# Performance work log

Measured on AMD Instinct MI355X. Metric: run time of the kernel, lower is better.

## Reference

```python
import jax, jax.numpy as jnp
import numpy as np

N = 100000      # n_nodes
D = 64          # in_features == out_features (elementwise W mul requires equality)
DEG = 16        # avg degree for random edges
H = 2           # n_head
ALPHA = 0.2     # LeakyReLU negative slope


def setup_inputs() -> dict:
    key = jax.random.key(0)
    k1, k2, k3 = jax.random.split(key, 3)
    inputs = jax.random.normal(k1, (N, D), dtype=jnp.float32)
    # random edges + self-loops so every row has at least one edge (nonzero rowsum)
    rnd = jax.random.randint(k2, (2, N * DEG), 0, N)
    self_loops = jnp.tile(jnp.arange(N)[None, :], (2, 1))
    edge_index = jnp.concatenate([self_loops, rnd], axis=1)  # [2, 1.7M]
    # per-head params, matching torch init: W = ones, a ~ U(-stdv, stdv)
    W = jnp.ones((H, D), dtype=jnp.float32)
    stdv = 1.0 / np.sqrt(D * 2)
    a = jax.random.uniform(k3, (H, 2 * D), dtype=jnp.float32, minval=-stdv, maxval=stdv)
    return {"inputs": inputs, "edge_index": edge_index, "W": W, "a": a}


def reference(inputs, edge_index, W, a):
    n = inputs.shape[0]
    row, col = edge_index[0], edge_index[1]

    def head(Wh, ah):
        h = inputs * Wh  # [N, D]
        # a @ [h_src; h_dst] decomposes into per-node dots, then scalar edge gather
        score = (h @ ah[:D])[row] + (h @ ah[D:])[col]          # [E]
        e = jnp.exp(jnp.where(score > 0, score, ALPHA * score))  # exp(leaky_relu)
        rowsum = jax.ops.segment_sum(e, row, num_segments=n)     # [N]
        # sparse.mm(coo(edge, e), inputs): h_prime[i] = sum_j e_ij * inputs[j]
        h_prime = jax.ops.segment_sum(e[:, None] * inputs[col], row, num_segments=n)
        return h_prime / rowsum[:, None]

    outs = jax.vmap(head)(W, a)  # [H, N, D]
    return outs.mean(axis=0)
```

## Files before the change

kernel.cpp:

```cpp
#include <hip/hip_runtime.h>


#define D 64
#define ALPHA 0.2f
#define CAP 96
#define BSHIFT 9
#define BROWS 512
#define MAXBUK 256
#define TILE 2048
#define PACKSHIFT 23
#define COLMASK ((1u << PACKSHIFT) - 1u)

__device__ __forceinline__ unsigned bf16rne(float f) {
    unsigned u = __float_as_uint(f);
    u += 0x7fffu + ((u >> 16) & 1u);
    return u >> 16;
}

__global__ __launch_bounds__(256) void k_scores_cast(
    const float* __restrict__ x, const float* __restrict__ W,
    const float* __restrict__ a, float4* __restrict__ s,
    unsigned short* __restrict__ xh, int N)
{
    int wid  = (blockIdx.x * blockDim.x + threadIdx.x) >> 6;
    int lane = threadIdx.x & 63;
    if (wid >= N) return;
    float v = x[(size_t)wid * D + lane];
    xh[(size_t)wid * D + lane] = (unsigned short)bf16rne(v);
    float h0 = v * W[lane];
    float h1 = v * W[D + lane];
    float t0 = h0 * a[lane];
    float t1 = h0 * a[D + lane];
    float t2 = h1 * a[2 * D + lane];
    float t3 = h1 * a[3 * D + lane];
#pragma unroll
    for (int off = 32; off; off >>= 1) {
        t0 += __shfl_xor(t0, off);
        t1 += __shfl_xor(t1, off);
        t2 += __shfl_xor(t2, off);
        t3 += __shfl_xor(t3, off);
    }
    if (lane == 0) s[wid] = make_float4(t0, t1, t2, t3);
}

__global__ __launch_bounds__(256) void k_tile_hist(
    const int* __restrict__ row, unsigned short* __restrict__ tcnt, int E, int nbuk)
{
    __shared__ int h[MAXBUK];
    int t = threadIdx.x, base = blockIdx.x * TILE;
    int cnt = E - base; if (cnt > TILE) cnt = TILE;
    for (int i = t; i < nbuk; i += 256) h[i] = 0;
    __syncthreads();
    for (int i = t; i < cnt; i += 256) atomicAdd(&h[row[base + i] >> BSHIFT], 1);
    __syncthreads();
    for (int i = t; i < nbuk; i += 256)
        tcnt[(size_t)blockIdx.x * MAXBUK + i] = (unsigned short)h[i];
}

__global__ __launch_bounds__(256) void k_col_scan(
    const unsigned short* __restrict__ tcnt, int* __restrict__ tbase,
    int* __restrict__ bcnt, int NT, int nbuk)
{
    __shared__ int wsum[256];
    int b = blockIdx.x, t = threadIdx.x;
    int t4 = t * 4;
    int v0 = (t4     < NT) ? tcnt[(size_t)(t4    ) * MAXBUK + b] : 0;
    int v1 = (t4 + 1 < NT) ? tcnt[(size_t)(t4 + 1) * MAXBUK + b] : 0;
    int v2 = (t4 + 2 < NT) ? tcnt[(size_t)(t4 + 2) * MAXBUK + b] : 0;
    int v3 = (t4 + 3 < NT) ? tcnt[(size_t)(t4 + 3) * MAXBUK + b] : 0;
    int sv = v0 + v1 + v2 + v3;
    wsum[t] = sv;
    __syncthreads();
    for (int off = 1; off < 256; off <<= 1) {
        int add = (t >= off) ? wsum[t - off] : 0;
        __syncthreads();
        wsum[t] += add;
        __syncthreads();
    }
    int run = wsum[t] - sv;
    if (t4     < NT) { tbase[(t4    ) * MAXBUK + b] = run; run += v0; }
    if (t4 + 1 < NT) { tbase[(t4 + 1) * MAXBUK + b] = run; run += v1; }
    if (t4 + 2 < NT) { tbase[(t4 + 2) * MAXBUK + b] = run; run += v2; }
    if (t4 + 3 < NT) { tbase[(t4 + 3) * MAXBUK + b] = run; run += v3; }
    if (t == 255) bcnt[b] = wsum[255];
}

__global__ void k_bucket_scan(const int* __restrict__ bcnt,
                              int* __restrict__ bbase, int nbuk)
{
    __shared__ int sd[MAXBUK];
    int t = threadIdx.x;
    int v = (t < nbuk) ? bcnt[t] : 0;
    sd[t] = v;
    __syncthreads();
    for (int off = 1; off < MAXBUK; off <<= 1) {
        int add = (t >= off) ? sd[t - off] : 0;
        __syncthreads();
        sd[t] += add;
        __syncthreads();
    }
    if (t < nbuk) bbase[t] = sd[t] - v;
    if (t == nbuk - 1) bbase[nbuk] = sd[t];
}

__global__ __launch_bounds__(256) void k_binning(
    const int* __restrict__ row, const int* __restrict__ col,
    const int* __restrict__ bbase, const int* __restrict__ tbase,
    unsigned* __restrict__ ebuf, int E, int nbuk)
{
    __shared__ int lrow[TILE];
    __shared__ int lcol[TILE];
    __shared__ int h[MAXBUK];
    __shared__ int st[MAXBUK];
    __shared__ int gb[MAXBUK];
    __shared__ int cur[MAXBUK];
    __shared__ int sd[MAXBUK];
    int t = threadIdx.x;
    int base = blockIdx.x * TILE;
    int cnt = E - base; if (cnt > TILE) cnt = TILE;

    for (int i = t; i < nbuk; i += 256) h[i] = 0;
    __syncthreads();

    int r[8], c[8], b[8];
#pragma unroll
    for (int j = 0; j < 8; j++) {
        int li = j * 256 + t;
        if (li < cnt) {
            int idx = base + li;
            r[j] = row[idx]; c[j] = col[idx]; b[j] = r[j] >> BSHIFT;
            atomicAdd(&h[b[j]], 1);
        } else b[j] = -1;
    }
    __syncthreads();

    sd[t] = (t < nbuk) ? h[t] : 0;
    __syncthreads();
    for (int off = 1; off < MAXBUK; off <<= 1) {
        int add = (t >= off) ? sd[t - off] : 0;
        __syncthreads();
        sd[t] += add;
        __syncthreads();
    }
    if (t < nbuk) {
        int start = sd[t] - h[t];
        st[t]  = start;
        cur[t] = start;
        gb[t]  = bbase[t] + tbase[blockIdx.x * MAXBUK + t];
    }
    __syncthreads();

#pragma unroll
    for (int j = 0; j < 8; j++) {
        if (b[j] >= 0) {
            int p = atomicAdd(&cur[b[j]], 1);
            lrow[p] = r[j]; lcol[p] = c[j];
        }
    }
    __syncthreads();

    for (int i = t; i < cnt; i += 256) {
        int rr = lrow[i];
        int bb = rr >> BSHIFT;
        ebuf[gb[bb] + (i - st[bb])] =
            ((unsigned)(rr & (BROWS - 1)) << PACKSHIFT) | (unsigned)lcol[i];
    }
}

__global__ __launch_bounds__(1024) void k_rowsort(
    const unsigned* __restrict__ ebuf, const int* __restrict__ bbase,
    int* __restrict__ offsets, int* __restrict__ counts,
    int* __restrict__ scol, int N)
{
    __shared__ int hist[BROWS];
    __shared__ int offs[BROWS];
    __shared__ int wsum[256];
    int b = blockIdx.x, t = threadIdx.x;
    int lo = b << BSHIFT;
    int s0 = bbase[b], s1 = bbase[b + 1];

    if (t < BROWS) hist[t] = 0;
    __syncthreads();
    for (int i = s0 + t; i < s1; i += 1024)
        atomicAdd(&hist[ebuf[i] >> PACKSHIFT], 1);
    __syncthreads();

    int a0 = 0, a1 = 0, sv = 0;
    if (t < 256) { a0 = hist[2 * t]; a1 = hist[2 * t + 1]; sv = a0 + a1; wsum[t] = sv; }
    __syncthreads();
    for (int off = 1; off < 256; off <<= 1) {
        int add = 0;
        if (t < 256 && t >= off) add = wsum[t - off];
        __syncthreads();
        if (t < 256) wsum[t] += add;
        __syncthreads();
    }
    if (t < 256) { int run = wsum[t] - sv; offs[2 * t] = run; offs[2 * t + 1] = run + a0; }
    __syncthreads();

    if (t < BROWS) {
        int rg = lo + t;
        if (rg < N) { offsets[rg] = s0 + offs[t]; counts[rg] = hist[t]; }
    }
    __syncthreads();
    if (t < BROWS) hist[t] = offs[t];
    __syncthreads();

    for (int i = s0 + t; i < s1; i += 1024) {
        unsigned pk = ebuf[i];
        int p = atomicAdd(&hist[pk >> PACKSHIFT], 1);
        scol[s0 + p] = (int)(pk & COLMASK);
    }
}

__global__ __launch_bounds__(256) void k_gather(
    const unsigned* __restrict__ xh2, const float4* __restrict__ s,
    const int* __restrict__ offsets, const int* __restrict__ counts,
    const int* __restrict__ scol, float* __restrict__ out, int N)
{
    __shared__ float  le0[4][CAP];
    __shared__ float  le1[4][CAP];
    __shared__ float2 lpair[4][CAP];
    int w    = threadIdx.x >> 6;
    int lane = threadIdx.x & 63;
    int n    = blockIdx.x * 4 + w;
    bool valid = (n < N);
    int start = 0, cnt = 0;
    float4 srow = make_float4(0.f, 0.f, 0.f, 0.f);
    if (valid) { start = offsets[n]; cnt = counts[n]; srow = s[n]; }

    float sum0 = 0.f, sum1 = 0.f;
    for (int k = lane; k < cnt; k += 64) {
        int c = scol[start + k];
        float4 sc = s[c];
        float sc0 = srow.x + sc.y;
        float sc1 = srow.z + sc.w;
        float e0 = __expf(sc0 > 0.f ? sc0 : ALPHA * sc0);
        float e1 = __expf(sc1 > 0.f ? sc1 : ALPHA * sc1);
        sum0 += e0; sum1 += e1;
        if (k < CAP) { lpair[w][k].x = __int_as_float(c); le0[w][k] = e0; le1[w][k] = e1; }
    }
    int m  = cnt < CAP ? cnt : CAP;
    int mp = (m + 7) & ~7;
    {
        int k = m + lane;
        if (k < mp) { lpair[w][k].x = __int_as_float(0); le0[w][k] = 0.f; le1[w][k] = 0.f; }
    }
#pragma unroll
    for (int off = 32; off; off >>= 1) {
        sum0 += __shfl_xor(sum0, off);
        sum1 += __shfl_xor(sum1, off);
    }
    if (!valid) return;
    float inv0 = 0.5f / sum0, inv1 = 0.5f / sum1;
    for (int k = lane; k < mp; k += 64)
        lpair[w][k].y = inv0 * le0[w][k] + inv1 * le1[w][k];

    int half = lane >> 5;
    int li   = lane & 31;
    float acc0 = 0.f, acc1 = 0.f;
    for (int k = 0; k < mp; k += 8) {
#pragma unroll
        for (int j = 0; j < 4; j++) {
            int kk = k + 2 * j + half;
            float2 pr = lpair[w][kk];
            int c = __float_as_int(pr.x);
            unsigned u = xh2[((unsigned)c << 5) + li];
            acc0 += pr.y * __uint_as_float(u << 16);
            acc1 += pr.y * __uint_as_float(u & 0xffff0000u);
        }
    }
    for (int kk = CAP + half; kk < cnt; kk += 2) {
        int c = scol[start + kk];
        float4 sc = s[c];
        float sc0 = srow.x + sc.y, sc1 = srow.z + sc.w;
        float coef = inv0 * __expf(sc0 > 0.f ? sc0 : ALPHA * sc0)
                   + inv1 * __expf(sc1 > 0.f ? sc1 : ALPHA * sc1);
        unsigned u = xh2[((unsigned)c << 5) + li];
        acc0 += coef * __uint_as_float(u << 16);
        acc1 += coef * __uint_as_float(u & 0xffff0000u);
    }
    acc0 += __shfl_xor(acc0, 32);
    acc1 += __shfl_xor(acc1, 32);
    if (half == 0) {
        float2* o = (float2*)(out + (size_t)n * D);
        o[li] = make_float2(acc0, acc1);
    }
}

extern "C" void kernel_launch(void* const* d_in, const int* in_sizes, int n_in,
                              void* d_out, int out_size, void* d_ws, size_t ws_size,
                              hipStream_t stream)
{
    const float* x  = (const float*)d_in[0];
    const int*   ei = (const int*)d_in[1];
    const float* W  = (const float*)d_in[2];
    const float* a  = (const float*)d_in[3];
    float*       out = (float*)d_out;
    int N = in_sizes[0] / D;
    int E = in_sizes[1] / 2;
    const int* row = ei;
    const int* col = ei + E;

    int NBUK = (N + BROWS - 1) >> BSHIFT;
    int NT   = (E + TILE - 1) / TILE;

    uintptr_t wp = (uintptr_t)d_ws;
    auto alloc = [&wp](size_t bytes) -> void* {
        wp = (wp + 255) & ~(uintptr_t)255;
        void* p = (void*)wp;
        wp += bytes;
        return p;
    };
    unsigned short* xh      = (unsigned short*)alloc((size_t)N * D * 2);
    float4*         s       = (float4*)alloc((size_t)N * sizeof(float4));
    int*            offsets = (int*)alloc((size_t)N * sizeof(int));
    int*            counts  = (int*)alloc((size_t)N * sizeof(int));
    int*            scol    = (int*)alloc((size_t)E * sizeof(int));
    unsigned*       ebuf    = (unsigned*)alloc((size_t)E * sizeof(unsigned));
    int*            tbase   = (int*)alloc((size_t)NT * MAXBUK * sizeof(int));
    int*            bcnt    = (int*)alloc(MAXBUK * sizeof(int));
    int*            bbase   = (int*)alloc((MAXBUK + 4) * sizeof(int));
    unsigned short* tcnt    = (unsigned short*)alloc((size_t)NT * MAXBUK * 2);

    k_scores_cast<<<(N + 3) / 4, 256, 0, stream>>>(x, W, a, s, xh, N);
    k_tile_hist<<<NT, 256, 0, stream>>>(row, tcnt, E, NBUK);
    k_col_scan<<<NBUK, 256, 0, stream>>>(tcnt, tbase, bcnt, NT, NBUK);
    k_bucket_scan<<<1, MAXBUK, 0, stream>>>(bcnt, bbase, NBUK);
    k_binning<<<NT, 256, 0, stream>>>(row, col, bbase, tbase, ebuf, E, NBUK);
    k_rowsort<<<NBUK, 1024, 0, stream>>>(ebuf, bbase, offsets, counts, scol, N);
    k_gather<<<(N + 3) / 4, 256, 0, stream>>>((const unsigned*)xh, s, offsets, counts, scol, out, N);
}
```

Measured before the change: 184.3 us.

## Fuse row sort with gather per bucket and merge front-end kernels

Merges score/cast and tile histogram into one launch, folds the bucket scan into the binning kernel, and replaces the separate rowsort plus per-row gather with a single per-bucket kernel. That kernel sorts edges in LDS, computes exp scores and rowsums once, and gathers features directly. This removes the scol/offsets/counts round trips through global memory, the recomputation of exponentials, and two launches. In exchange it stores exp values as fp16, shrinks buckets to 256 rows, packs column indices into 17 bits (limits N to 131072), and adds a slower fallback path for oversized buckets.

```diff
diff --git a/kernel.cpp b/kernel.cpp
--- a/kernel.cpp
+++ b/kernel.cpp
@@ -1,68 +1,81 @@
 #include <hip/hip_runtime.h>
+#include <hip/hip_fp16.h>
 
 
 #define D 64
 #define ALPHA 0.2f
-#define CAP 96
-#define BSHIFT 9
-#define BROWS 512
-#define MAXBUK 256
+#define BSHIFT 8
+#define BROWS 256
+#define MAXBUK 512
 #define TILE 2048
-#define PACKSHIFT 23
-#define COLMASK ((1u << PACKSHIFT) - 1u)
+#define PK2 17
+#define M17 ((1u << PK2) - 1u)
+#define CAPE 8192
 
 __device__ __forceinline__ unsigned bf16rne(float f) {
     unsigned u = __float_as_uint(f);
     u += 0x7fffu + ((u >> 16) & 1u);
     return u >> 16;
 }
-
-__global__ __launch_bounds__(256) void k_scores_cast(
+__device__ __forceinline__ unsigned packe(float e0, float e1) {
+    __half2 h = __floats2half2_rn(e0, e1);
+    return *reinterpret_cast<unsigned*>(&h);
+}
+__device__ __forceinline__ float2 unpacke(unsigned u) {
+    __half2 h = *reinterpret_cast<__half2*>(&u);
+    return __half22float2(h);
+}
+__device__ __forceinline__ float lrexp(float sc) {
+    return __expf(sc > 0.f ? sc : ALPHA * sc);
+}
+
+__global__ __launch_bounds__(256) void k_front(
     const float* __restrict__ x, const float* __restrict__ W,
     const float* __restrict__ a, float4* __restrict__ s,
-    unsigned short* __restrict__ xh, int N)
-{
-    int wid  = (blockIdx.x * blockDim.x + threadIdx.x) >> 6;
-    int lane = threadIdx.x & 63;
-    if (wid >= N) return;
-    float v = x[(size_t)wid * D + lane];
-    xh[(size_t)wid * D + lane] = (unsigned short)bf16rne(v);
-    float h0 = v * W[lane];
-    float h1 = v * W[D + lane];
-    float t0 = h0 * a[lane];
-    float t1 = h0 * a[D + lane];
-    float t2 = h1 * a[2 * D + lane];
-    float t3 = h1 * a[3 * D + lane];
+    unsigned short* __restrict__ xh, const int* __restrict__ row,
+    unsigned short* __restrict__ tcnt, int N, int E, int nblkA, int nbuk)
+{
+    __shared__ int h[MAXBUK];
+    if ((int)blockIdx.x < nblkA) {
+        int wid  = (blockIdx.x * 256 + threadIdx.x) >> 6;
+        int lane = threadIdx.x & 63;
+        if (wid >= N) return;
+        float v = x[(size_t)wid * D + lane];
+        xh[(size_t)wid * D + lane] = (unsigned short)bf16rne(v);
+        float h0 = v * W[lane];
+        float h1 = v * W[D + lane];
+        float t0 = h0 * a[lane];
+        float t1 = h0 * a[D + lane];
+        float t2 = h1 * a[2 * D + lane];
+        float t3 = h1 * a[3 * D + lane];
 #pragma unroll
-    for (int off = 32; off; off >>= 1) {
-        t0 += __shfl_xor(t0, off);
-        t1 += __shfl_xor(t1, off);
-        t2 += __shfl_xor(t2, off);
-        t3 += __shfl_xor(t3, off);
-    }
-    if (lane == 0) s[wid] = make_float4(t0, t1, t2, t3);
-}
-
-__global__ __launch_bounds__(256) void k_tile_hist(
-    const int* __restrict__ row, unsigned short* __restrict__ tcnt, int E, int nbuk)
-{
-    __shared__ int h[MAXBUK];
-    int t = threadIdx.x, base = blockIdx.x * TILE;
-    int cnt = E - base; if (cnt > TILE) cnt = TILE;
-    for (int i = t; i < nbuk; i += 256) h[i] = 0;
-    __syncthreads();
-    for (int i = t; i < cnt; i += 256) atomicAdd(&h[row[base + i] >> BSHIFT], 1);
-    __syncthreads();
-    for (int i = t; i < nbuk; i += 256)
-        tcnt[(size_t)blockIdx.x * MAXBUK + i] = (unsigned short)h[i];
+        for (int off = 32; off; off >>= 1) {
+            t0 += __shfl_xor(t0, off);
+            t1 += __shfl_xor(t1, off);
+            t2 += __shfl_xor(t2, off);
+            t3 += __shfl_xor(t3, off);
+        }
+        if (lane == 0) s[wid] = make_float4(t0, t1, t2, t3);
+    } else {
+        int tile = blockIdx.x - nblkA;
+        int t = threadIdx.x, base = tile * TILE;
+        int cnt = E - base; if (cnt > TILE) cnt = TILE;
+        h[t] = 0; h[t + 256] = 0;
+        __syncthreads();
+        for (int i = t; i < cnt; i += 256) atomicAdd(&h[row[base + i] >> BSHIFT], 1);
+        __syncthreads();
+        tcnt[(size_t)tile * MAXBUK + t]       = (unsigned short)h[t];
+        tcnt[(size_t)tile * MAXBUK + t + 256] = (unsigned short)h[t + 256];
+    }
 }
 
 __global__ __launch_bounds__(256) void k_col_scan(
     const unsigned short* __restrict__ tcnt, int* __restrict__ tbase,
     int* __restrict__ bcnt, int NT, int nbuk)
 {
+    int b = blockIdx.x, t = threadIdx.x;
+    if (b >= nbuk) { if (t == 0) bcnt[b] = 0; return; }
     __shared__ int wsum[256];
-    int b = blockIdx.x, t = threadIdx.x;
     int t4 = t * 4;
     int v0 = (t4     < NT) ? tcnt[(size_t)(t4    ) * MAXBUK + b] : 0;
     int v1 = (t4 + 1 < NT) ? tcnt[(size_t)(t4 + 1) * MAXBUK + b] : 0;
@@ -78,35 +91,17 @@
         __syncthreads();
     }
     int run = wsum[t] - sv;
-    if (t4     < NT) { tbase[(t4    ) * MAXBUK + b] = run; run += v0; }
-    if (t4 + 1 < NT) { tbase[(t4 + 1) * MAXBUK + b] = run; run += v1; }
-    if (t4 + 2 < NT) { tbase[(t4 + 2) * MAXBUK + b] = run; run += v2; }
-    if (t4 + 3 < NT) { tbase[(t4 + 3) * MAXBUK + b] = run; run += v3; }
+    if (t4     < NT) { tbase[(size_t)(t4    ) * MAXBUK + b] = run; run += v0; }
+    if (t4 + 1 < NT) { tbase[(size_t)(t4 + 1) * MAXBUK + b] = run; run += v1; }
+    if (t4 + 2 < NT) { tbase[(size_t)(t4 + 2) * MAXBUK + b] = run; run += v2; }
+    if (t4 + 3 < NT) { tbase[(size_t)(t4 + 3) * MAXBUK + b] = run; run += v3; }
     if (t == 255) bcnt[b] = wsum[255];
-}
-
-__global__ void k_bucket_scan(const int* __restrict__ bcnt,
-                              int* __restrict__ bbase, int nbuk)
-{
-    __shared__ int sd[MAXBUK];
-    int t = threadIdx.x;
-    int v = (t < nbuk) ? bcnt[t] : 0;
-    sd[t] = v;
-    __syncthreads();
-    for (int off = 1; off < MAXBUK; off <<= 1) {
-        int add = (t >= off) ? sd[t - off] : 0;
-        __syncthreads();
-        sd[t] += add;
-        __syncthreads();
-    }
-    if (t < nbuk) bbase[t] = sd[t] - v;
-    if (t == nbuk - 1) bbase[nbuk] = sd[t];
 }
 
 __global__ __launch_bounds__(256) void k_binning(
     const int* __restrict__ row, const int* __restrict__ col,
-    const int* __restrict__ bbase, const int* __restrict__ tbase,
-    unsigned* __restrict__ ebuf, int E, int nbuk)
+    const int* __restrict__ bcnt, const int* __restrict__ tbase,
+    unsigned* __restrict__ ebuf, int* __restrict__ bbase_g, int E, int nbuk)
 {
     __shared__ int lrow[TILE];
     __shared__ int lcol[TILE];
@@ -114,12 +109,12 @@
     __shared__ int st[MAXBUK];
     __shared__ int gb[MAXBUK];
     __shared__ int cur[MAXBUK];
-    __shared__ int sd[MAXBUK];
+    __shared__ int w2[256];
     int t = threadIdx.x;
     int base = blockIdx.x * TILE;
     int cnt = E - base; if (cnt > TILE) cnt = TILE;
 
-    for (int i = t; i < nbuk; i += 256) h[i] = 0;
+    h[t] = 0; h[t + 256] = 0;
     __syncthreads();
 
     int r[8], c[8], b[8];
@@ -134,19 +129,37 @@
     }
     __syncthreads();
 
-    sd[t] = (t < nbuk) ? h[t] : 0;
-    __syncthreads();
-    for (int off = 1; off < MAXBUK; off <<= 1) {
-        int add = (t >= off) ? sd[t - off] : 0;
-        __syncthreads();
-        sd[t] += add;
-        __syncthreads();
-    }
-    if (t < nbuk) {
-        int start = sd[t] - h[t];
-        st[t]  = start;
-        cur[t] = start;
-        gb[t]  = bbase[t] + tbase[blockIdx.x * MAXBUK + t];
+    int a0 = h[2 * t], a1 = h[2 * t + 1];
+    int sv = a0 + a1;
+    w2[t] = sv;
+    __syncthreads();
+    for (int off = 1; off < 256; off <<= 1) {
+        int add = (t >= off) ? w2[t - off] : 0;
+        __syncthreads();
+        w2[t] += add;
+        __syncthreads();
+    }
+    int run = w2[t] - sv;
+    st[2 * t] = run;        st[2 * t + 1] = run + a0;
+    cur[2 * t] = run;       cur[2 * t + 1] = run + a0;
+    __syncthreads();
+
+    int b0 = bcnt[2 * t], b1 = bcnt[2 * t + 1];
+    int sb = b0 + b1;
+    w2[t] = sb;
+    __syncthreads();
+    for (int off = 1; off < 256; off <<= 1) {
+        int add = (t >= off) ? w2[t - off] : 0;
+        __syncthreads();
+        w2[t] += add;
+        __syncthreads();
+    }
+    int runb = w2[t] - sb;
+    gb[2 * t]     = runb      + tbase[(size_t)blockIdx.x * MAXBUK + 2 * t];
+    gb[2 * t + 1] = runb + b0 + tbase[(size_t)blockIdx.x * MAXBUK + 2 * t + 1];
+    if (blockIdx.x == 0) {
+        bbase_g[2 * t] = runb; bbase_g[2 * t + 1] = runb + b0;
+        if (t == 255) bbase_g[512] = runb + b0 + b1;
     }
     __syncthreads();
 
@@ -163,128 +176,179 @@
         int rr = lrow[i];
         int bb = rr >> BSHIFT;
         ebuf[gb[bb] + (i - st[bb])] =
-            ((unsigned)(rr & (BROWS - 1)) << PACKSHIFT) | (unsigned)lcol[i];
-    }
-}
-
-__global__ __launch_bounds__(1024) void k_rowsort(
+            ((unsigned)(rr & (BROWS - 1)) << PK2) | (unsigned)lcol[i];
+    }
+}
+
+__global__ __launch_bounds__(512) void k_bucket_gather(
+    const unsigned* __restrict__ xh2, const float4* __restrict__ s,
     const unsigned* __restrict__ ebuf, const int* __restrict__ bbase,
-    int* __restrict__ offsets, int* __restrict__ counts,
-    int* __restrict__ scol, int N)
-{
-    __shared__ int hist[BROWS];
-    __shared__ int offs[BROWS];
-    __shared__ int wsum[256];
+    float* __restrict__ out, int N)
+{
+    __shared__ unsigned pkA[CAPE];
+    __shared__ unsigned evA[CAPE];
+    __shared__ int   hist[BROWS];
+    __shared__ int   offs[BROWS + 1];
+    __shared__ int   cursor[BROWS];
+    __shared__ float rs0[BROWS], rs1[BROWS];
+    __shared__ float rsx[BROWS], rsz[BROWS];
+    __shared__ int   wsum[256];
     int b = blockIdx.x, t = threadIdx.x;
     int lo = b << BSHIFT;
     int s0 = bbase[b], s1 = bbase[b + 1];
-
-    if (t < BROWS) hist[t] = 0;
-    __syncthreads();
-    for (int i = s0 + t; i < s1; i += 1024)
-        atomicAdd(&hist[ebuf[i] >> PACKSHIFT], 1);
-    __syncthreads();
-
-    int a0 = 0, a1 = 0, sv = 0;
-    if (t < 256) { a0 = hist[2 * t]; a1 = hist[2 * t + 1]; sv = a0 + a1; wsum[t] = sv; }
-    __syncthreads();
-    for (int off = 1; off < 256; off <<= 1) {
-        int add = 0;
-        if (t < 256 && t >= off) add = wsum[t - off];
-        __syncthreads();
-        if (t < 256) wsum[t] += add;
-        __syncthreads();
-    }
-    if (t < 256) { int run = wsum[t] - sv; offs[2 * t] = run; offs[2 * t + 1] = run + a0; }
-    __syncthreads();
+    int seg = s1 - s0;
 
     if (t < BROWS) {
-        int rg = lo + t;
-        if (rg < N) { offsets[rg] = s0 + offs[t]; counts[rg] = hist[t]; }
-    }
-    __syncthreads();
-    if (t < BROWS) hist[t] = offs[t];
-    __syncthreads();
-
-    for (int i = s0 + t; i < s1; i += 1024) {
-        unsigned pk = ebuf[i];
-        int p = atomicAdd(&hist[pk >> PACKSHIFT], 1);
-        scol[s0 + p] = (int)(pk & COLMASK);
-    }
-}
-
-__global__ __launch_bounds__(256) void k_gather(
-    const unsigned* __restrict__ xh2, const float4* __restrict__ s,
-    const int* __restrict__ offsets, const int* __restrict__ counts,
-    const int* __restrict__ scol, float* __restrict__ out, int N)
-{
-    __shared__ float  le0[4][CAP];
-    __shared__ float  le1[4][CAP];
-    __shared__ float2 lpair[4][CAP];
-    int w    = threadIdx.x >> 6;
-    int lane = threadIdx.x & 63;
-    int n    = blockIdx.x * 4 + w;
-    bool valid = (n < N);
-    int start = 0, cnt = 0;
-    float4 srow = make_float4(0.f, 0.f, 0.f, 0.f);
-    if (valid) { start = offsets[n]; cnt = counts[n]; srow = s[n]; }
-
-    float sum0 = 0.f, sum1 = 0.f;
-    for (int k = lane; k < cnt; k += 64) {
-        int c = scol[start + k];
-        float4 sc = s[c];
-        float sc0 = srow.x + sc.y;
-        float sc1 = srow.z + sc.w;
-        float e0 = __expf(sc0 > 0.f ? sc0 : ALPHA * sc0);
-        float e1 = __expf(sc1 > 0.f ? sc1 : ALPHA * sc1);
-        sum0 += e0; sum1 += e1;
-        if (k < CAP) { lpair[w][k].x = __int_as_float(c); le0[w][k] = e0; le1[w][k] = e1; }
-    }
-    int m  = cnt < CAP ? cnt : CAP;
-    int mp = (m + 7) & ~7;
-    {
-        int k = m + lane;
-        if (k < mp) { lpair[w][k].x = __int_as_float(0); le0[w][k] = 0.f; le1[w][k] = 0.f; }
-    }
-#pragma unroll
-    for (int off = 32; off; off >>= 1) {
-        sum0 += __shfl_xor(sum0, off);
-        sum1 += __shfl_xor(sum1, off);
-    }
-    if (!valid) return;
-    float inv0 = 0.5f / sum0, inv1 = 0.5f / sum1;
-    for (int k = lane; k < mp; k += 64)
-        lpair[w][k].y = inv0 * le0[w][k] + inv1 * le1[w][k];
-
-    int half = lane >> 5;
-    int li   = lane & 31;
-    float acc0 = 0.f, acc1 = 0.f;
-    for (int k = 0; k < mp; k += 8) {
-#pragma unroll
-        for (int j = 0; j < 4; j++) {
-            int kk = k + 2 * j + half;
-            float2 pr = lpair[w][kk];
-            int c = __float_as_int(pr.x);
-            unsigned u = xh2[((unsigned)c << 5) + li];
-            acc0 += pr.y * __uint_as_float(u << 16);
-            acc1 += pr.y * __uint_as_float(u & 0xffff0000u);
-        }
-    }
-    for (int kk = CAP + half; kk < cnt; kk += 2) {
-        int c = scol[start + kk];
-        float4 sc = s[c];
-        float sc0 = srow.x + sc.y, sc1 = srow.z + sc.w;
-        float coef = inv0 * __expf(sc0 > 0.f ? sc0 : ALPHA * sc0)
-                   + inv1 * __expf(sc1 > 0.f ? sc1 : ALPHA * sc1);
-        unsigned u = xh2[((unsigned)c << 5) + li];
-        acc0 += coef * __uint_as_float(u << 16);
-        acc1 += coef * __uint_as_float(u & 0xffff0000u);
-    }
-    acc0 += __shfl_xor(acc0, 32);
-    acc1 += __shfl_xor(acc1, 32);
-    if (half == 0) {
-        float2* o = (float2*)(out + (size_t)n * D);
-        o[li] = make_float2(acc0, acc1);
+        int g = lo + t;
+        float4 f = (g < N) ? s[g] : make_float4(0.f, 0.f, 0.f, 0.f);
+        rsx[t] = f.x; rsz[t] = f.z;
+        hist[t] = 0; rs0[t] = 0.f; rs1[t] = 0.f;
+    }
+    __syncthreads();
+
+    if (seg <= CAPE) {
+        for (int i = s0 + t; i < s1; i += 512)
+            atomicAdd(&hist[ebuf[i] >> PK2], 1);
+        __syncthreads();
+        int a = 0;
+        if (t < BROWS) { a = hist[t]; wsum[t] = a; }
+        __syncthreads();
+        for (int off = 1; off < 256; off <<= 1) {
+            int add = 0;
+            if (t < BROWS && t >= off) add = wsum[t - off];
+            __syncthreads();
+            if (t < BROWS) wsum[t] += add;
+            __syncthreads();
+        }
+        if (t < BROWS) {
+            offs[t] = wsum[t] - a; cursor[t] = wsum[t] - a;
+            if (t == BROWS - 1) offs[BROWS] = wsum[t];
+        }
+        __syncthreads();
+        for (int i = s0 + t; i < s1; i += 512) {
+            unsigned pk = ebuf[i];
+            int r = pk >> PK2, c = (int)(pk & M17);
+            float4 sc = s[c];
+            float e0 = lrexp(rsx[r] + sc.y);
+            float e1 = lrexp(rsz[r] + sc.w);
+            atomicAdd(&rs0[r], e0);
+            atomicAdd(&rs1[r], e1);
+            int p = atomicAdd(&cursor[r], 1);
+            pkA[p] = pk; evA[p] = packe(e0, e1);
+        }
+        __syncthreads();
+        if (t < BROWS) { rs0[t] = 0.5f / rs0[t]; rs1[t] = 0.5f / rs1[t]; }
+        __syncthreads();
+        for (int i = t; i < seg; i += 512) {
+            unsigned pk = pkA[i];
+            int r = pk >> PK2;
+            float2 ef = unpacke(evA[i]);
+            evA[i] = __float_as_uint(rs0[r] * ef.x + rs1[r] * ef.y);
+        }
+        __syncthreads();
+
+        int wv = t >> 6, lane = t & 63, half = lane >> 5, li = lane & 31;
+        for (int j = 0; j < 32; j++) {
+            int r = wv * 32 + j;
+            int g = lo + r;
+            if (g >= N) continue;
+            int st2 = offs[r], en = offs[r + 1];
+            float acc0 = 0.f, acc1 = 0.f;
+            int kk = st2 + half;
+            for (; kk + 2 < en; kk += 4) {
+                unsigned pka = pkA[kk],   pkb = pkA[kk + 2];
+                float ca = __uint_as_float(evA[kk]);
+                float cb = __uint_as_float(evA[kk + 2]);
+                unsigned ua = xh2[(((unsigned)(pka & M17)) << 5) + li];
+                unsigned ub = xh2[(((unsigned)(pkb & M17)) << 5) + li];
+                acc0 += ca * __uint_as_float(ua << 16);
+                acc1 += ca * __uint_as_float(ua & 0xffff0000u);
+                acc0 += cb * __uint_as_float(ub << 16);
+                acc1 += cb * __uint_as_float(ub & 0xffff0000u);
+            }
+            for (; kk < en; kk += 2) {
+                unsigned pk = pkA[kk];
+                float cf = __uint_as_float(evA[kk]);
+                unsigned u = xh2[(((unsigned)(pk & M17)) << 5) + li];
+                acc0 += cf * __uint_as_float(u << 16);
+                acc1 += cf * __uint_as_float(u & 0xffff0000u);
+            }
+            acc0 += __shfl_xor(acc0, 32);
+            acc1 += __shfl_xor(acc1, 32);
+            if (half == 0)
+                ((float2*)(out + (size_t)g * D))[li] = make_float2(acc0, acc1);
+        }
+    } else {
+        for (int i = s0 + t; i < s1; i += 512) {
+            unsigned pk = ebuf[i];
+            int r = pk >> PK2, c = (int)(pk & M17);
+            float4 sc = s[c];
+            atomicAdd(&rs0[r], lrexp(rsx[r] + sc.y));
+            atomicAdd(&rs1[r], lrexp(rsz[r] + sc.w));
+        }
+        __syncthreads();
+        if (t < BROWS) { rs0[t] = 0.5f / rs0[t]; rs1[t] = 0.5f / rs1[t]; }
+        for (int idx = t; idx < BROWS * D; idx += 512) {
+            int g = lo + (idx >> 6);
+            if (g < N) out[(size_t)g * D + (idx & 63)] = 0.f;
+        }
+        __syncthreads();
+        for (int base = s0; base < s1; base += CAPE) {
+            int ce = base + CAPE; if (ce > s1) ce = s1;
+            if (t < BROWS) hist[t] = 0;
+            __syncthreads();
+            for (int i = base + t; i < ce; i += 512)
+                atomicAdd(&hist[ebuf[i] >> PK2], 1);
+            __syncthreads();
+            int a = 0;
+            if (t < BROWS) { a = hist[t]; wsum[t] = a; }
+            __syncthreads();
+            for (int off = 1; off < 256; off <<= 1) {
+                int add = 0;
+                if (t < BROWS && t >= off) add = wsum[t - off];
+                __syncthreads();
+                if (t < BROWS) wsum[t] += add;
+                __syncthreads();
+            }
+            if (t < BROWS) {
+                offs[t] = wsum[t] - a; cursor[t] = wsum[t] - a;
+                if (t == BROWS - 1) offs[BROWS] = wsum[t];
+            }
+            __syncthreads();
+            for (int i = base + t; i < ce; i += 512) {
+                unsigned pk = ebuf[i];
+                int r = pk >> PK2, c = (int)(pk & M17);
+                float4 sc = s[c];
+                float coef = rs0[r] * lrexp(rsx[r] + sc.y)
+                           + rs1[r] * lrexp(rsz[r] + sc.w);
+                int p = atomicAdd(&cursor[r], 1);
+                pkA[p] = pk; evA[p] = __float_as_uint(coef);
+            }
+            __syncthreads();
+            int wv = t >> 6, lane = t & 63, half = lane >> 5, li = lane & 31;
+            for (int j = 0; j < 32; j++) {
+                int r = wv * 32 + j;
+                int g = lo + r;
+                if (g >= N) continue;
+                int st2 = offs[r], en = offs[r + 1];
+                float acc0 = 0.f, acc1 = 0.f;
+                for (int kk = st2 + half; kk < en; kk += 2) {
+                    unsigned pk = pkA[kk];
+                    float cf = __uint_as_float(evA[kk]);
+                    unsigned u = xh2[(((unsigned)(pk & M17)) << 5) + li];
+                    acc0 += cf * __uint_as_float(u << 16);
+                    acc1 += cf * __uint_as_float(u & 0xffff0000u);
+                }
+                acc0 += __shfl_xor(acc0, 32);
+                acc1 += __shfl_xor(acc1, 32);
+                if (half == 0) {
+                    float2* o = (float2*)(out + (size_t)g * D);
+                    float2 old = o[li];
+                    o[li] = make_float2(old.x + acc0, old.y + acc1);
+                }
+            }
+            __syncthreads();
+        }
     }
 }
 
@@ -312,22 +376,17 @@
         wp += bytes;
         return p;
     };
-    unsigned short* xh      = (unsigned short*)alloc((size_t)N * D * 2);
-    float4*         s       = (float4*)alloc((size_t)N * sizeof(float4));
-    int*            offsets = (int*)alloc((size_t)N * sizeof(int));
-    int*            counts  = (int*)alloc((size_t)N * sizeof(int));
-    int*            scol    = (int*)alloc((size_t)E * sizeof(int));
-    unsigned*       ebuf    = (unsigned*)alloc((size_t)E * sizeof(unsigned));
-    int*            tbase   = (int*)alloc((size_t)NT * MAXBUK * sizeof(int));
-    int*            bcnt    = (int*)alloc(MAXBUK * sizeof(int));
-    int*            bbase   = (int*)alloc((MAXBUK + 4) * sizeof(int));
-    unsigned short* tcnt    = (unsigned short*)alloc((size_t)NT * MAXBUK * 2);
-
-    k_scores_cast<<<(N + 3) / 4, 256, 0, stream>>>(x, W, a, s, xh, N);
-    k_tile_hist<<<NT, 256, 0, stream>>>(row, tcnt, E, NBUK);
-    k_col_scan<<<NBUK, 256, 0, stream>>>(tcnt, tbase, bcnt, NT, NBUK);
-    k_bucket_scan<<<1, MAXBUK, 0, stream>>>(bcnt, bbase, NBUK);
-    k_binning<<<NT, 256, 0, stream>>>(row, col, bbase, tbase, ebuf, E, NBUK);
-    k_rowsort<<<NBUK, 1024, 0, stream>>>(ebuf, bbase, offsets, counts, scol, N);
-    k_gather<<<(N + 3) / 4, 256, 0, stream>>>((const unsigned*)xh, s, offsets, counts, scol, out, N);
-}
+    unsigned short* xh    = (unsigned short*)alloc((size_t)N * D * 2);
+    float4*         s     = (float4*)alloc((size_t)N * sizeof(float4));
+    unsigned*       ebuf  = (unsigned*)alloc((size_t)E * sizeof(unsigned));
+    int*            tbase = (int*)alloc((size_t)NT * MAXBUK * sizeof(int));
+    int*            bcnt  = (int*)alloc(MAXBUK * sizeof(int));
+    int*            bbase = (int*)alloc((MAXBUK + 4) * sizeof(int));
+    unsigned short* tcnt  = (unsigned short*)alloc((size_t)NT * MAXBUK * 2);
+
+    int nblkA = (N + 3) / 4;
+    k_front<<<nblkA + NT, 256, 0, stream>>>(x, W, a, s, xh, row, tcnt, N, E, nblkA, NBUK);
+    k_col_scan<<<MAXBUK, 256, 0, stream>>>(tcnt, tbase, bcnt, NT, NBUK);
+    k_binning<<<NT, 256, 0, stream>>>(row, col, bcnt, tbase, ebuf, bbase, E, NBUK);
+    k_bucket_gather<<<NBUK, 512, 0, stream>>>((const unsigned*)xh, s, ebuf, bbase, out, N);
+}
```

New measurement: 229.6 us. +24.6%, slower.
